# Kernel optimization log

Measured on AMD Instinct MI355X. Metric: run time of the kernel, lower is better.

## Reference

```python
import jax, jax.numpy as jnp
import numpy as np


def setup_inputs() -> dict:
    key = jax.random.key(0)
    ks = jax.random.split(key, 8)
    B, N, F, H, D, C = 16, 8192, 512, 512, 256, 2
    s = 0.02
    return {
        "h": jax.random.normal(ks[0], (B, N, F), dtype=jnp.float32),
        "W1": jax.random.normal(ks[1], (F, H), dtype=jnp.float32) * s,
        "b1": jnp.zeros((H,), jnp.float32),
        "Wa": jax.random.normal(ks[2], (H, D), dtype=jnp.float32) * s,
        "ba": jnp.zeros((D,), jnp.float32),
        "Wb": jax.random.normal(ks[3], (H, D), dtype=jnp.float32) * s,
        "bb": jnp.zeros((D,), jnp.float32),
        "Wc": jax.random.normal(ks[4], (D, 1), dtype=jnp.float32) * s,
        "bc": jnp.zeros((1,), jnp.float32),
        "Wcls": jax.random.normal(ks[5], (H, C), dtype=jnp.float32) * s,
        "bcls": jnp.zeros((C,), jnp.float32),
    }


def reference(h, W1, b1, Wa, ba, Wb, bb, Wc, bc, Wcls, bcls):
    # h: [B, N, F]  (B bags, N instances each)
    h1 = jax.nn.relu(jnp.einsum("bnf,fh->bnh", h, W1) + b1)        # [B,N,H]
    a = jnp.tanh(jnp.einsum("bnh,hd->bnd", h1, Wa) + ba)           # [B,N,D]
    g = jax.nn.sigmoid(jnp.einsum("bnh,hd->bnd", h1, Wb) + bb)     # [B,N,D]
    A = jnp.einsum("bnd,dk->bnk", a * g, Wc) + bc                  # [B,N,1]
    A_raw = jnp.swapaxes(A, 1, 2)                                  # [B,1,N]
    A_sm = jax.nn.softmax(A_raw, axis=-1)                          # [B,1,N]
    M = jnp.einsum("bkn,bnh->bkh", A_sm, h1)                       # [B,1,H]
    context = jnp.mean(M, axis=0)                                  # [1,H]  (sum / len(h_list))
    logits = context @ Wcls + bcls                                 # [1,C]
    Y_prob = jax.nn.softmax(logits, axis=1)
    Y_hat = jnp.argmax(logits, axis=1, keepdims=True)
    return (logits, Y_prob, Y_hat, A_raw, M)
```

## Files before the change

kernel.cpp:

```cpp
#include <hip/hip_runtime.h>
#include <math.h>

typedef short bf16x8 __attribute__((ext_vector_type(8)));
typedef float f32x4  __attribute__((ext_vector_type(4)));

#define GLOAD_LDS16(SRC, DST) \
  __builtin_amdgcn_global_load_lds((const __attribute__((address_space(1))) void*)(SRC), \
      (__attribute__((address_space(3))) void*)(DST), 16, 0, 0)

#define WAITVM(N) asm volatile("s_waitcnt vmcnt(" #N ")" ::: "memory")
#define WAITLGKM0 asm volatile("s_waitcnt lgkmcnt(0)" ::: "memory")
#define BARRIER() do { __builtin_amdgcn_s_barrier(); asm volatile("" ::: "memory"); } while (0)

__device__ __forceinline__ unsigned short f2bf(float f) {
  union { float f; unsigned u; } v; v.f = f;
  unsigned r = v.u + 0x7FFFu + ((v.u >> 16) & 1u);
  return (unsigned short)(r >> 16);
}
__device__ __forceinline__ float bf2f(unsigned short s) {
  union { unsigned u; float f; } v; v.u = ((unsigned)s) << 16;
  return v.f;
}
__device__ __forceinline__ unsigned pk2bf(float lo, float hi) {
  unsigned r;
  asm("v_cvt_pk_bf16_f32 %0, %1, %2" : "=v"(r) : "v"(lo), "v"(hi));
  return r;
}
__device__ __forceinline__ float fexp2(float x) {
  float r; asm("v_exp_f32 %0, %1" : "=v"(r) : "v"(x)); return r;
}
__device__ __forceinline__ float frcp(float x) {
  float r; asm("v_rcp_f32 %0, %1" : "=v"(r) : "v"(x)); return r;
}
#define LOG2E 1.44269504f
__device__ __forceinline__ float fexp(float x) { return fexp2(x * LOG2E); }


__global__ void carp_wpack(const float* __restrict__ W1, const float* __restrict__ Wa,
                           const float* __restrict__ Wb,
                           unsigned short* __restrict__ W1T_pk, unsigned short* __restrict__ WabT_pk) {
  int t = blockIdx.x * 256 + threadIdx.x;
  int mat = t >> 15;
  int gid = t & 32767;
  int g = gid & 511;
  int kt = (gid >> 9) & 15;
  int p = gid >> 13;
  int s = g >> 6, l = g & 63;
  int j = p * 128 + s * 16 + (l & 15);
  int k = kt * 32 + (l >> 4) * 8;
  unsigned short v[8];
  if (mat == 0) {
#pragma unroll
    for (int e = 0; e < 8; ++e) v[e] = f2bf(W1[(size_t)(k + e) * 512 + j]);
    *(uint4*)(W1T_pk + (size_t)gid * 8) = *(const uint4*)v;
  } else {
    int d = j >> 1;
    const float* Wx = (j & 1) ? Wb : Wa;
#pragma unroll
    for (int e = 0; e < 8; ++e) v[e] = f2bf(Wx[(size_t)(k + e) * 256 + d]);
    *(uint4*)(WabT_pk + (size_t)gid * 8) = *(const uint4*)v;
  }
}

__launch_bounds__(512, 2)
__global__ void carp_gemm1(const float* __restrict__ h, const unsigned short* __restrict__ W1T_pk,
                           const float* __restrict__ b1, unsigned short* __restrict__ h1_pk) {
  __shared__ __align__(16) unsigned short lds[65536];
  int bid0 = blockIdx.x;
  int bid = (bid0 & 7) * 128 + (bid0 >> 3);
  int bn = bid & 1, bm = bid >> 1;
  int brow = bm * 256;
  int tid = threadIdx.x, lane = tid & 63, wid = tid >> 6;
  int wr = wid >> 1, wc = wid & 1;

  f32x4 acc[4][8] = {};
  float4 ar[8];

  int r0 = tid >> 4;
  int chunk = tid & 15;
  const float* hbase = h + (size_t)(brow + r0) * 512 + chunk * 4;
  int kgA = (chunk & 7) >> 1, r16A = r0 & 15;
  int aw_const = (chunk >> 3) * 8192 + (r0 >> 4) * 1024 + kgA * 256
               + ((r16A * 16) ^ (kgA << 5) ^ ((chunk >> 3) << 4)) + (chunk & 1) * 8;
  int aread_lane = (lane >> 4) * 256 + (((lane & 15) * 16) ^ ((lane >> 4) << 5));

#define G1_LOADA(TP) do { \
  _Pragma("unroll") for (int q = 0; q < 8; ++q) \
    ar[q] = *(const float4*)(hbase + (size_t)(q * 32) * 512 + (TP) * 64); \
  } while (0)
#define G1_WRITEA(TP) do { \
  char* dstA = (char*)lds + ((TP) & 1) * 32768; \
  _Pragma("unroll") for (int q = 0; q < 8; ++q) { \
    uint2 wv; wv.x = pk2bf(ar[q].x, ar[q].y); wv.y = pk2bf(ar[q].z, ar[q].w); \
    *(uint2*)(dstA + (q >> 2) * 16384 + (q & 3) * 2048 + aw_const) = wv; \
  } } while (0)
#define G1_STAGEB(TP, BUF) do { \
  _Pragma("unroll") for (int q = 0; q < 4; ++q) { \
    int c = wid * 4 + q; \
    int pn = 2 * bn + ((c & 15) >> 3); \
    GLOAD_LDS16(W1T_pk + ((size_t)(pn * 16 + (TP) * 2 + (c >> 4)) * 512 + (c & 7) * 64 + lane) * 8, \
                (char*)lds + 65536 + (BUF) * 32768 + (size_t)c * 1024); \
  } } while (0)

  G1_LOADA(0);
  WAITVM(0);
  G1_WRITEA(0);
  G1_STAGEB(0, 0);
  G1_LOADA(1);
  WAITLGKM0;

#pragma unroll 1
  for (int tp = 0; tp < 8; ++tp) {
    if (tp < 7) G1_STAGEB(tp + 1, (tp + 1) & 1);
    if (tp < 7) { WAITVM(12); } else { WAITVM(0); }
    BARRIER();
    const char* Abase = (const char*)lds + (tp & 1) * 32768;
    const char* Bbase = (const char*)lds + 65536 + (tp & 1) * 32768;
#pragma unroll
    for (int tt = 0; tt < 2; ++tt) {
      bf16x8 afr[4], bfr[8];
#pragma unroll
      for (int m = 0; m < 4; ++m) {
        int gs = wr * 4 + m;
        afr[m] = *(const bf16x8*)(Abase + (gs >> 3) * 16384 + tt * 8192
                                  + (gs & 7) * 1024 + (aread_lane ^ (tt << 4)));
      }
#pragma unroll
      for (int n = 0; n < 8; ++n)
        bfr[n] = *(const bf16x8*)(Bbase + tt * 16384 + wc * 8192
                                  + (size_t)(n * 64 + lane) * 16);
#pragma unroll
      for (int m = 0; m < 4; ++m)
#pragma unroll
        for (int n = 0; n < 8; ++n)
          acc[m][n] = __builtin_amdgcn_mfma_f32_16x16x32_bf16(afr[m], bfr[n], acc[m][n], 0, 0, 0);
    }
    if (tp < 7) { WAITVM(4); G1_WRITEA(tp + 1); }
    if (tp < 6) G1_LOADA(tp + 2);
    WAITLGKM0;
    BARRIER();
  }
#undef G1_LOADA
#undef G1_WRITEA
#undef G1_STAGEB

  unsigned short* img = lds;
#pragma unroll
  for (int n = 0; n < 8; ++n) {
    int cl = wc * 128 + n * 16 + (lane & 15);
    float bias = b1[bn * 256 + cl];
    int ktc = cl >> 5, c32 = cl & 31;
#pragma unroll
    for (int m = 0; m < 4; ++m)
#pragma unroll
      for (int j = 0; j < 4; ++j) {
        int r = wr * 64 + m * 16 + (lane >> 4) * 4 + j;
        float v = acc[m][n][j] + bias;
        v = v > 0.f ? v : 0.f;
        int gidx = (r >> 7) * 4096 + ktc * 512 + ((r & 127) >> 4) * 64 + (c32 >> 3) * 16 + (r & 15);
        img[(size_t)gidx * 8 + (c32 & 7)] = f2bf(v);
      }
  }
  __syncthreads();
#pragma unroll
  for (int i = 0; i < 16; ++i) {
    int g = i * 512 + tid;
    int P = (2 * bm + (g >> 12)) * 16 + bn * 8 + ((g >> 9) & 7);
    *(uint4*)(h1_pk + ((size_t)P * 512 + (g & 511)) * 8) = *(const uint4*)(img + (size_t)g * 8);
  }
}

#define G2_STAGE(T32, HALF, BUF) do { \
  _Pragma("unroll") for (int q = 0; q < 2; ++q) { \
    int c = wid * 2 + q; \
    int P = (2 * bm + (c >> 3)) * 16 + (T32); \
    GLOAD_LDS16(h1_pk + ((size_t)P * 512 + (c & 7) * 64 + lane) * 8, \
                (char*)lds + (BUF) * 32768 + (HALF) * 16384 + (size_t)c * 1024); \
  } \
  _Pragma("unroll") for (int q = 0; q < 2; ++q) { \
    int c2 = wid * 2 + q; \
    int pn = 2 * bn + (c2 >> 3); \
    GLOAD_LDS16(WabT_pk + ((size_t)(pn * 16 + (T32)) * 512 + (c2 & 7) * 64 + lane) * 8, \
                (char*)lds + 65536 + (BUF) * 32768 + (HALF) * 16384 + (size_t)c2 * 1024); \
  } } while (0)

__launch_bounds__(512, 2)
__global__ void carp_gemm2(const unsigned short* __restrict__ h1_pk, const unsigned short* __restrict__ WabT_pk,
                           const float* __restrict__ ba, const float* __restrict__ bb,
                           const float* __restrict__ Wc, float* __restrict__ A_part) {
  __shared__ __align__(16) unsigned short lds[65536];
  int bid0 = blockIdx.x;
  int bid = (bid0 & 7) * 128 + (bid0 >> 3);
  int bn = bid & 1, bm = bid >> 1;
  int tid = threadIdx.x, lane = tid & 63, wid = tid >> 6;
  int wr = wid >> 1, wc = wid & 1;

  f32x4 acc[4][8] = {};

  G2_STAGE(0, 0, 0); G2_STAGE(1, 1, 0);

#pragma unroll 1
  for (int kt = 0; kt < 8; ++kt) {
    int cur = kt & 1, nxt = cur ^ 1;
    if (kt < 7) { G2_STAGE(2 * kt + 2, 0, nxt); G2_STAGE(2 * kt + 3, 1, nxt); }
    if (kt < 7) { WAITVM(8); } else { WAITVM(0); }
    BARRIER();
#pragma unroll
    for (int tt = 0; tt < 2; ++tt) {
      const char* Ab = (const char*)lds + cur * 32768 + tt * 16384;
      const char* Bb = (const char*)lds + 65536 + cur * 32768 + tt * 16384 + wc * 8192;
      bf16x8 afr[4], bfr[8];
#pragma unroll
      for (int m = 0; m < 4; ++m)
        afr[m] = *(const bf16x8*)(Ab + (size_t)((wr * 4 + m) * 64 + lane) * 16);
#pragma unroll
      for (int n = 0; n < 8; ++n)
        bfr[n] = *(const bf16x8*)(Bb + (size_t)(n * 64 + lane) * 16);
#pragma unroll
      for (int m = 0; m < 4; ++m)
#pragma unroll
        for (int n = 0; n < 8; ++n)
          acc[m][n] = __builtin_amdgcn_mfma_f32_16x16x32_bf16(afr[m], bfr[n], acc[m][n], 0, 0, 0);
    }
    WAITLGKM0;
    BARRIER();
  }

  int brow = bm * 256, bcol = bn * 256;
  int odd = lane & 1;
  float kA = odd ? -LOG2E : -2.f * LOG2E;
  float c1 = odd ? 1.f : 2.f;
  float c0 = odd ? 0.f : -1.f;
  float rowpart[4][4] = {};
#pragma unroll
  for (int n = 0; n < 8; ++n) {
    int cg = bcol + wc * 128 + n * 16 + (lane & 15);
    int d = cg >> 1;
    float bias = (cg & 1) ? bb[d] : ba[d];
    float wcd = Wc[d];
#pragma unroll
    for (int m = 0; m < 4; ++m)
#pragma unroll
      for (int j = 0; j < 4; ++j) {
        float v = acc[m][n][j] + bias;
        float av = c1 * frcp(1.f + fexp2(kA * v)) + c0;
        float pv = av * __shfl_xor(av, 1, 64);
        rowpart[m][j] += pv * wcd;
      }
  }
#pragma unroll
  for (int m = 0; m < 4; ++m)
#pragma unroll
    for (int j = 0; j < 4; ++j) {
      float t = rowpart[m][j];
      t += __shfl_xor(t, 2, 64);
      t += __shfl_xor(t, 4, 64);
      t += __shfl_xor(t, 8, 64);
      rowpart[m][j] = t;
    }
  if ((lane & 15) == 0) {
    int slot = bn * 2 + wc;
#pragma unroll
    for (int m = 0; m < 4; ++m)
#pragma unroll
      for (int j = 0; j < 4; ++j) {
        int row = brow + wr * 64 + m * 16 + (lane >> 4) * 4 + j;
        A_part[(size_t)row * 4 + slot] = rowpart[m][j];
      }
  }
}
#undef G2_STAGE

__global__ void carp_softmax(const float* __restrict__ A_part, const float* __restrict__ bc,
                             float* __restrict__ A_raw_out, float* __restrict__ A_sm) {
  __shared__ float sv[8192];
  __shared__ float red[256];
  int b = blockIdx.x, tid = threadIdx.x;
  float bcv = bc[0];
  float lmax = -1e30f;
  for (int i = tid; i < 8192; i += 256) {
    float4 x = *(const float4*)(A_part + (size_t)(b * 8192 + i) * 4);
    float s = (x.x + x.y) + (x.z + x.w) + bcv;
    sv[i] = s;
    A_raw_out[b * 8192 + i] = s;
    lmax = fmaxf(lmax, s);
  }
  red[tid] = lmax;
  for (int s = 128; s > 0; s >>= 1) { __syncthreads(); if (tid < s) red[tid] = fmaxf(red[tid], red[tid + s]); }
  __syncthreads();
  float mx = red[0];
  __syncthreads();
  float lsum = 0.f;
  for (int i = tid; i < 8192; i += 256) {
    float e = fexp(sv[i] - mx);
    sv[i] = e;
    lsum += e;
  }
  red[tid] = lsum;
  for (int s = 128; s > 0; s >>= 1) { __syncthreads(); if (tid < s) red[tid] += red[tid + s]; }
  __syncthreads();
  float inv = 1.f / red[0];
  for (int i = tid; i < 8192; i += 256) A_sm[b * 8192 + i] = sv[i] * inv;
}

__global__ void carp_mkernel(const unsigned short* __restrict__ h1_pk, const float* __restrict__ A_sm,
                             float* __restrict__ Mpart) {
  __shared__ float sw[128];
  int bm = blockIdx.x;
  int tid = threadIdx.x;
  if (tid < 128) sw[tid] = A_sm[bm * 128 + tid];
  __syncthreads();
  int l = tid & 63;
  float acc[4][8] = {};
#pragma unroll
  for (int tq = 0; tq < 4; ++tq) {
    int tt = (tid >> 6) * 4 + tq;
#pragma unroll
    for (int s = 0; s < 8; ++s) {
      const unsigned short* gp = h1_pk + ((size_t)(bm * 16 + tt) * 512 + s * 64 + l) * 8;
      uint4 raw = *(const uint4*)gp;
      const unsigned short* pv = (const unsigned short*)&raw;
      float w = sw[s * 16 + (l & 15)];
#pragma unroll
      for (int e = 0; e < 8; ++e) acc[tq][e] += w * bf2f(pv[e]);
    }
  }
#pragma unroll
  for (int tq = 0; tq < 4; ++tq)
#pragma unroll
    for (int e = 0; e < 8; ++e) {
      float t = acc[tq][e];
      t += __shfl_xor(t, 1, 64);
      t += __shfl_xor(t, 2, 64);
      t += __shfl_xor(t, 4, 64);
      t += __shfl_xor(t, 8, 64);
      acc[tq][e] = t;
    }
  if ((l & 15) == 0) {
    int cc = (l >> 4) & 3;
#pragma unroll
    for (int tq = 0; tq < 4; ++tq) {
      int tt = (tid >> 6) * 4 + tq;
      float* mp = Mpart + (size_t)bm * 512 + tt * 32 + cc * 8;
#pragma unroll
      for (int e = 0; e < 8; ++e) mp[e] = acc[tq][e];
    }
  }
}

__global__ void carp_final(const float* __restrict__ Mpart, const float* __restrict__ Wcls,
                           const float* __restrict__ bcls, float* __restrict__ out) {
  __shared__ float ctx[512];
  int t = threadIdx.x;
  float c = 0.f;
  for (int b = 0; b < 16; ++b) {
    float s = 0.f;
    for (int p = 0; p < 64; ++p) s += Mpart[((size_t)(b * 64 + p) << 9) + t];
    out[131077 + b * 512 + t] = s;
    c += s;
  }
  ctx[t] = c * (1.f / 16.f);
  __syncthreads();
  if (t < 64) {
    float p0 = 0.f, p1 = 0.f;
    for (int hh = t; hh < 512; hh += 64) {
      float cv = ctx[hh];
      p0 += cv * Wcls[hh * 2];
      p1 += cv * Wcls[hh * 2 + 1];
    }
    for (int m = 1; m < 64; m <<= 1) { p0 += __shfl_xor(p0, m, 64); p1 += __shfl_xor(p1, m, 64); }
    if (t == 0) {
      float l0 = p0 + bcls[0], l1 = p1 + bcls[1];
      out[0] = l0; out[1] = l1;
      float mx = fmaxf(l0, l1);
      float e0 = expf(l0 - mx), e1 = expf(l1 - mx);
      float s = e0 + e1;
      out[2] = e0 / s; out[3] = e1 / s;
      out[4] = (l1 > l0) ? 1.0f : 0.0f;
    }
  }
}

extern "C" void kernel_launch(void* const* d_in, const int* in_sizes, int n_in,
                              void* d_out, int out_size, void* d_ws, size_t ws_size,
                              hipStream_t stream) {
  const float* h    = (const float*)d_in[0];
  const float* W1   = (const float*)d_in[1];
  const float* b1   = (const float*)d_in[2];
  const float* Wa   = (const float*)d_in[3];
  const float* ba   = (const float*)d_in[4];
  const float* Wb   = (const float*)d_in[5];
  const float* bb   = (const float*)d_in[6];
  const float* Wc   = (const float*)d_in[7];
  const float* bc   = (const float*)d_in[8];
  const float* Wcls = (const float*)d_in[9];
  const float* bcls = (const float*)d_in[10];
  float* out = (float*)d_out;

  char* ws = (char*)d_ws;
  unsigned short* h1_pk   = (unsigned short*)(ws);
  unsigned short* W1T_pk  = (unsigned short*)(ws + 134217728);
  unsigned short* WabT_pk = (unsigned short*)(ws + 134742016);
  float* A_part           = (float*)(ws + 135266304);
  float* A_sm             = (float*)(ws + 139460608);
  float* Mpart            = (float*)(ws + 135266304);

  carp_wpack  <<<256,  256, 0, stream>>>(W1, Wa, Wb, W1T_pk, WabT_pk);
  carp_gemm1  <<<1024, 512, 0, stream>>>(h, W1T_pk, b1, h1_pk);
  carp_gemm2  <<<1024, 512, 0, stream>>>(h1_pk, WabT_pk, ba, bb, Wc, A_part);
  carp_softmax<<<16,   256, 0, stream>>>(A_part, bc, out + 5, A_sm);
  carp_mkernel<<<1024, 256, 0, stream>>>(h1_pk, A_sm, Mpart);
  carp_final  <<<1,    512, 0, stream>>>(Mpart, Wcls, bcls, out);
}
```

Before: 310.9 us.

## Load weight B fragments directly from global memory into registers, skipping LDS

In both GEMM kernels the weight (B) operand is no longer staged through LDS with global_load_lds. Each wave now reads its packed bf16 fragments straight from global memory (expected to be L2-resident) into registers just before the MFMAs. Without B staging, the end-of-iteration barrier is dropped, the A write/prefetch is moved to just after the top barrier, and gemm2's LDS allocation is halved. The aim is less LDS traffic and fewer synchronisations per K step. The cost is that global-load latency for B is exposed inside the compute loop with no prefetch, and the vmcnt wait counts now depend on compiler-inserted waits.

```diff
diff --git a/kernel.cpp b/kernel.cpp
--- a/kernel.cpp
+++ b/kernel.cpp
@@ -72,6 +72,7 @@
   int brow = bm * 256;
   int tid = threadIdx.x, lane = tid & 63, wid = tid >> 6;
   int wr = wid >> 1, wc = wid & 1;
+  int pn = 2 * bn + wc;
 
   f32x4 acc[4][8] = {};
   float4 ar[8];
@@ -94,31 +95,26 @@
     uint2 wv; wv.x = pk2bf(ar[q].x, ar[q].y); wv.y = pk2bf(ar[q].z, ar[q].w); \
     *(uint2*)(dstA + (q >> 2) * 16384 + (q & 3) * 2048 + aw_const) = wv; \
   } } while (0)
-#define G1_STAGEB(TP, BUF) do { \
-  _Pragma("unroll") for (int q = 0; q < 4; ++q) { \
-    int c = wid * 4 + q; \
-    int pn = 2 * bn + ((c & 15) >> 3); \
-    GLOAD_LDS16(W1T_pk + ((size_t)(pn * 16 + (TP) * 2 + (c >> 4)) * 512 + (c & 7) * 64 + lane) * 8, \
-                (char*)lds + 65536 + (BUF) * 32768 + (size_t)c * 1024); \
-  } } while (0)
 
   G1_LOADA(0);
   WAITVM(0);
   G1_WRITEA(0);
-  G1_STAGEB(0, 0);
   G1_LOADA(1);
   WAITLGKM0;
 
 #pragma unroll 1
   for (int tp = 0; tp < 8; ++tp) {
-    if (tp < 7) G1_STAGEB(tp + 1, (tp + 1) & 1);
-    if (tp < 7) { WAITVM(12); } else { WAITVM(0); }
+    if (tp == 0) { WAITVM(0); } else { WAITVM(16); }
     BARRIER();
+    if (tp < 7) G1_WRITEA(tp + 1);
+    if (tp < 6) G1_LOADA(tp + 2);
     const char* Abase = (const char*)lds + (tp & 1) * 32768;
-    const char* Bbase = (const char*)lds + 65536 + (tp & 1) * 32768;
 #pragma unroll
     for (int tt = 0; tt < 2; ++tt) {
       bf16x8 afr[4], bfr[8];
+#pragma unroll
+      for (int n = 0; n < 8; ++n)
+        bfr[n] = *(const bf16x8*)(W1T_pk + ((size_t)(pn * 16 + tp * 2 + tt) * 512 + n * 64 + lane) * 8);
 #pragma unroll
       for (int m = 0; m < 4; ++m) {
         int gs = wr * 4 + m;
@@ -126,23 +122,16 @@
                                   + (gs & 7) * 1024 + (aread_lane ^ (tt << 4)));
       }
 #pragma unroll
-      for (int n = 0; n < 8; ++n)
-        bfr[n] = *(const bf16x8*)(Bbase + tt * 16384 + wc * 8192
-                                  + (size_t)(n * 64 + lane) * 16);
-#pragma unroll
       for (int m = 0; m < 4; ++m)
 #pragma unroll
         for (int n = 0; n < 8; ++n)
           acc[m][n] = __builtin_amdgcn_mfma_f32_16x16x32_bf16(afr[m], bfr[n], acc[m][n], 0, 0, 0);
     }
-    if (tp < 7) { WAITVM(4); G1_WRITEA(tp + 1); }
-    if (tp < 6) G1_LOADA(tp + 2);
     WAITLGKM0;
-    BARRIER();
   }
 #undef G1_LOADA
 #undef G1_WRITEA
-#undef G1_STAGEB
+  BARRIER();
 
   unsigned short* img = lds;
 #pragma unroll
@@ -170,61 +159,55 @@
   }
 }
 
-#define G2_STAGE(T32, HALF, BUF) do { \
+__launch_bounds__(512, 2)
+__global__ void carp_gemm2(const unsigned short* __restrict__ h1_pk, const unsigned short* __restrict__ WabT_pk,
+                           const float* __restrict__ ba, const float* __restrict__ bb,
+                           const float* __restrict__ Wc, float* __restrict__ A_part) {
+  __shared__ __align__(16) unsigned short lds[32768];
+  int bid0 = blockIdx.x;
+  int bid = (bid0 & 7) * 128 + (bid0 >> 3);
+  int bn = bid & 1, bm = bid >> 1;
+  int tid = threadIdx.x, lane = tid & 63, wid = tid >> 6;
+  int wr = wid >> 1, wc = wid & 1;
+  int pn = 2 * bn + wc;
+
+  f32x4 acc[4][8] = {};
+
+#define G2_STAGE_A(T32, HALF, BUF) do { \
   _Pragma("unroll") for (int q = 0; q < 2; ++q) { \
     int c = wid * 2 + q; \
     int P = (2 * bm + (c >> 3)) * 16 + (T32); \
     GLOAD_LDS16(h1_pk + ((size_t)P * 512 + (c & 7) * 64 + lane) * 8, \
                 (char*)lds + (BUF) * 32768 + (HALF) * 16384 + (size_t)c * 1024); \
-  } \
-  _Pragma("unroll") for (int q = 0; q < 2; ++q) { \
-    int c2 = wid * 2 + q; \
-    int pn = 2 * bn + (c2 >> 3); \
-    GLOAD_LDS16(WabT_pk + ((size_t)(pn * 16 + (T32)) * 512 + (c2 & 7) * 64 + lane) * 8, \
-                (char*)lds + 65536 + (BUF) * 32768 + (HALF) * 16384 + (size_t)c2 * 1024); \
   } } while (0)
 
-__launch_bounds__(512, 2)
-__global__ void carp_gemm2(const unsigned short* __restrict__ h1_pk, const unsigned short* __restrict__ WabT_pk,
-                           const float* __restrict__ ba, const float* __restrict__ bb,
-                           const float* __restrict__ Wc, float* __restrict__ A_part) {
-  __shared__ __align__(16) unsigned short lds[65536];
-  int bid0 = blockIdx.x;
-  int bid = (bid0 & 7) * 128 + (bid0 >> 3);
-  int bn = bid & 1, bm = bid >> 1;
-  int tid = threadIdx.x, lane = tid & 63, wid = tid >> 6;
-  int wr = wid >> 1, wc = wid & 1;
-
-  f32x4 acc[4][8] = {};
-
-  G2_STAGE(0, 0, 0); G2_STAGE(1, 1, 0);
+  G2_STAGE_A(0, 0, 0); G2_STAGE_A(1, 1, 0);
 
 #pragma unroll 1
   for (int kt = 0; kt < 8; ++kt) {
     int cur = kt & 1, nxt = cur ^ 1;
-    if (kt < 7) { G2_STAGE(2 * kt + 2, 0, nxt); G2_STAGE(2 * kt + 3, 1, nxt); }
-    if (kt < 7) { WAITVM(8); } else { WAITVM(0); }
+    if (kt == 0) { WAITVM(0); } else { WAITVM(16); }
     BARRIER();
+    if (kt < 7) { G2_STAGE_A(2 * kt + 2, 0, nxt); G2_STAGE_A(2 * kt + 3, 1, nxt); }
 #pragma unroll
     for (int tt = 0; tt < 2; ++tt) {
       const char* Ab = (const char*)lds + cur * 32768 + tt * 16384;
-      const char* Bb = (const char*)lds + 65536 + cur * 32768 + tt * 16384 + wc * 8192;
       bf16x8 afr[4], bfr[8];
+#pragma unroll
+      for (int n = 0; n < 8; ++n)
+        bfr[n] = *(const bf16x8*)(WabT_pk + ((size_t)(pn * 16 + 2 * kt + tt) * 512 + n * 64 + lane) * 8);
 #pragma unroll
       for (int m = 0; m < 4; ++m)
         afr[m] = *(const bf16x8*)(Ab + (size_t)((wr * 4 + m) * 64 + lane) * 16);
 #pragma unroll
-      for (int n = 0; n < 8; ++n)
-        bfr[n] = *(const bf16x8*)(Bb + (size_t)(n * 64 + lane) * 16);
-#pragma unroll
       for (int m = 0; m < 4; ++m)
 #pragma unroll
         for (int n = 0; n < 8; ++n)
           acc[m][n] = __builtin_amdgcn_mfma_f32_16x16x32_bf16(afr[m], bfr[n], acc[m][n], 0, 0, 0);
     }
     WAITLGKM0;
-    BARRIER();
-  }
+  }
+#undef G2_STAGE_A
 
   int brow = bm * 256, bcol = bn * 256;
   int odd = lane & 1;
@@ -269,7 +252,6 @@
       }
   }
 }
-#undef G2_STAGE
 
 __global__ void carp_softmax(const float* __restrict__ A_part, const float* __restrict__ bc,
                              float* __restrict__ A_raw_out, float* __restrict__ A_sm) {
```

New measurement: 349.9 us. +12.5%, slower.
